# Performance work log

Measured on AMD Instinct MI355X. Metric: run time of the kernel, lower is better.

Reference implementation:

```python
import jax, jax.numpy as jnp
import numpy as np

D, H, W = 96, 160, 160
N_FLOWS = 3
RANGE_FLOW = 0.4


def make_base_grid():
    # torch.meshgrid over arange per dim, stacked: [1, 3, D, H, W], channel order (d, h, w)
    zz, yy, xx = jnp.meshgrid(jnp.arange(D), jnp.arange(H), jnp.arange(W), indexing='ij')
    return jnp.stack([zz, yy, xx]).astype(jnp.float32)[None]


def normalize_grid(g):
    # g: [1,3,D,H,W] voxel coords (d,h,w). Apply 2*(v/(s-1) - 0.5), permute to
    # channels-last and reverse channel order -> (x,y,z) as grid_sample expects.
    scale = jnp.array([2.0 / (D - 1), 2.0 / (H - 1), 2.0 / (W - 1)], jnp.float32).reshape(1, 3, 1, 1, 1)
    g = g * scale - 1.0
    return jnp.moveaxis(g, 1, -1)[..., ::-1]  # [1,D,H,W,3], xyz


def grid_sample_3d(img, grid):
    # Trilinear grid_sample, align_corners=False, zeros padding (torch defaults).
    # img: [N,C,D,H,W]; grid: [N,D,H,W,3] with (x,y,z) in [-1,1].
    N, C, Di, Hi, Wi = img.shape
    x = ((grid[..., 0] + 1.0) * Wi - 1.0) * 0.5
    y = ((grid[..., 1] + 1.0) * Hi - 1.0) * 0.5
    z = ((grid[..., 2] + 1.0) * Di - 1.0) * 0.5
    x0 = jnp.floor(x); y0 = jnp.floor(y); z0 = jnp.floor(z)
    tx = x - x0; ty = y - y0; tz = z - z0
    x0i = x0.astype(jnp.int32); y0i = y0.astype(jnp.int32); z0i = z0.astype(jnp.int32)

    gather = jax.vmap(lambda im, a, b, c: im[:, a, b, c])  # per-batch [C,D,H,W] gather

    out = jnp.zeros((N, C) + x.shape[1:], img.dtype)
    for dz in (0, 1):
        for dy in (0, 1):
            for dx in (0, 1):
                xi = x0i + dx; yi = y0i + dy; zi = z0i + dz
                w = ((tx if dx else 1.0 - tx) * (ty if dy else 1.0 - ty) * (tz if dz else 1.0 - tz))
                valid = ((xi >= 0) & (xi < Wi) & (yi >= 0) & (yi < Hi) & (zi >= 0) & (zi < Di))
                xi = jnp.clip(xi, 0, Wi - 1); yi = jnp.clip(yi, 0, Hi - 1); zi = jnp.clip(zi, 0, Di - 1)
                vals = gather(img, zi, yi, xi)  # [N,C,D,H,W]
                out = out + vals * (w * valid)[:, None]
    return out


def setup_inputs() -> dict:
    key = jax.random.key(0)
    k1, k2, k3 = jax.random.split(key, 3)
    src = jax.random.normal(k1, (1, 1, D, H, W), jnp.float32)
    flow_list = jax.random.normal(k2, (N_FLOWS, 1, 3, D, H, W), jnp.float32)
    final_flow = jax.random.normal(k3, (1, 3, D, H, W), jnp.float32)
    range_flow = jnp.float32(RANGE_FLOW)
    return {"src": src, "flow_list": flow_list, "final_flow": final_flow, "range_flow": range_flow}


def reference(src, flow_list, final_flow, range_flow):
    base = make_base_grid()  # [1,3,D,H,W]
    flows = [flow_list[i] for i in range(flow_list.shape[0])] + [final_flow]
    composed = flows[0]
    warped = composed
    for dvf in flows[1:]:
        grid2 = normalize_grid(base + dvf * range_flow)
        warped = grid_sample_3d(composed, grid2)  # warp running composition by dvf
        composed = warped + dvf
    out_flow = warped + final_flow  # == final composed dvf
    new_locs = normalize_grid(base + composed * range_flow)
    deform_2_img = grid_sample_3d(src, new_locs)
    return (deform_2_img, out_flow)
```

## Files before the change

### kernel.cpp

```cpp
#include <hip/hip_runtime.h>

constexpr int Dd  = 96;
constexpr int Hh  = 160;
constexpr int Ww  = 160;
constexpr int HW  = Hh * Ww;
constexpr int DHW = Dd * HW;

__device__ __forceinline__ float remap_z(float v) { return v * ((float)Dd / (float)(Dd - 1)) - 0.5f; }
__device__ __forceinline__ float remap_y(float v) { return v * ((float)Hh / (float)(Hh - 1)) - 0.5f; }
__device__ __forceinline__ float remap_x(float v) { return v * ((float)Ww / (float)(Ww - 1)) - 0.5f; }

__device__ __forceinline__ void tri_setup(float x, float y, float z,
                                          int off[8], float wgt[8]) {
    float xf = floorf(x), yf = floorf(y), zf = floorf(z);
    float tx = x - xf, ty = y - yf, tz = z - zf;
    int x0 = (int)xf, y0 = (int)yf, z0 = (int)zf;
    float wx[2] = {1.0f - tx, tx};
    float wy[2] = {1.0f - ty, ty};
    float wz[2] = {1.0f - tz, tz};
    int k = 0;
#pragma unroll
    for (int dz = 0; dz < 2; ++dz) {
        int zi = z0 + dz;
        bool vz = (zi >= 0) && (zi < Dd);
        int zc = min(max(zi, 0), Dd - 1);
#pragma unroll
        for (int dy = 0; dy < 2; ++dy) {
            int yi = y0 + dy;
            bool vy = (yi >= 0) && (yi < Hh);
            int yc = min(max(yi, 0), Hh - 1);
#pragma unroll
            for (int dx = 0; dx < 2; ++dx) {
                int xi = x0 + dx;
                bool vx = (xi >= 0) && (xi < Ww);
                int xc = min(max(xi, 0), Ww - 1);
                float w = wz[dz] * wy[dy] * wx[dx];
                wgt[k] = (vx && vy && vz) ? w : 0.0f;
                off[k] = zc * HW + yc * Ww + xc;
                ++k;
            }
        }
    }
}

__global__ __launch_bounds__(256) void pack3to4(
        const float* __restrict__ f, float4* __restrict__ out)
{
    int idx = blockIdx.x * blockDim.x + threadIdx.x;
    if (idx >= DHW) return;
    out[idx] = make_float4(f[idx], f[DHW + idx], f[2 * DHW + idx], 0.0f);
}

template <bool PLANAR_OUT>
__global__ __launch_bounds__(256) void warp_compose4(
        const float4* __restrict__ composed,
        const float* __restrict__ dvf,
        const float* __restrict__ rf_ptr,
        float* __restrict__ outp,
        float4* __restrict__ out4)
{
    int idx = blockIdx.x * blockDim.x + threadIdx.x;
    if (idx >= DHW) return;
    float rf = *rf_ptr;

    int d = idx / HW;
    int rem = idx - d * HW;
    int h = rem / Ww;
    int w = rem - h * Ww;

    float fd = dvf[idx];
    float fh = dvf[DHW + idx];
    float fw = dvf[2 * DHW + idx];

    float z = remap_z((float)d + fd * rf);
    float y = remap_y((float)h + fh * rf);
    float x = remap_x((float)w + fw * rf);

    int off[8]; float wgt[8];
    tri_setup(x, y, z, off, wgt);

    float a0 = 0.0f, a1 = 0.0f, a2 = 0.0f;
#pragma unroll
    for (int k = 0; k < 8; ++k) {
        float4 v = composed[off[k]];
        float wk = wgt[k];
        a0 += wk * v.x;
        a1 += wk * v.y;
        a2 += wk * v.z;
    }
    if (PLANAR_OUT) {
        outp[idx]           = a0 + fd;
        outp[DHW + idx]     = a1 + fh;
        outp[2 * DHW + idx] = a2 + fw;
    } else {
        out4[idx] = make_float4(a0 + fd, a1 + fh, a2 + fw, 0.0f);
    }
}

__global__ __launch_bounds__(256) void warp_src(
        const float* __restrict__ src,
        const float* __restrict__ composed,
        const float* __restrict__ rf_ptr,
        float* __restrict__ out)
{
    int idx = blockIdx.x * blockDim.x + threadIdx.x;
    if (idx >= DHW) return;
    float rf = *rf_ptr;

    int d = idx / HW;
    int rem = idx - d * HW;
    int h = rem / Ww;
    int w = rem - h * Ww;

    float fd = composed[idx];
    float fh = composed[DHW + idx];
    float fw = composed[2 * DHW + idx];

    float z = remap_z((float)d + fd * rf);
    float y = remap_y((float)h + fh * rf);
    float x = remap_x((float)w + fw * rf);

    int off[8]; float wgt[8];
    tri_setup(x, y, z, off, wgt);

    float acc = 0.0f;
#pragma unroll
    for (int k = 0; k < 8; ++k) {
        acc += wgt[k] * src[off[k]];
    }
    out[idx] = acc;
}

extern "C" void kernel_launch(void* const* d_in, const int* in_sizes, int n_in,
                              void* d_out, int out_size, void* d_ws, size_t ws_size,
                              hipStream_t stream) {
    const float* src        = (const float*)d_in[0];
    const float* flow_list  = (const float*)d_in[1];
    const float* final_flow = (const float*)d_in[2];
    const float* rf         = (const float*)d_in[3];

    float* out_img  = (float*)d_out;
    float* out_flow = (float*)d_out + DHW;

    float4* bufA = (float4*)d_ws;
    float4* bufB = bufA + DHW;

    const float* f0 = flow_list;
    const float* f1 = flow_list + 3 * (size_t)DHW;
    const float* f2 = flow_list + 6 * (size_t)DHW;

    dim3 block(256);
    dim3 grid(DHW / 256);

    pack3to4<<<grid, block, 0, stream>>>(f0, bufA);
    warp_compose4<false><<<grid, block, 0, stream>>>(bufA, f1, rf, nullptr, bufB);
    warp_compose4<false><<<grid, block, 0, stream>>>(bufB, f2, rf, nullptr, bufA);
    warp_compose4<true><<<grid, block, 0, stream>>>(bufA, final_flow, rf, out_flow, nullptr);
    warp_src<<<grid, block, 0, stream>>>(src, out_flow, rf, out_img);
}
```

Baseline: 294.5 us.

## Fuse final flow composition with source warp and swizzle block order

Merges the last compose step and the image warp into one kernel, so the composed flow is used from registers instead of being written out and read back, and one launch goes away. Block indices are also remapped so that consecutive workgroups are spread across eight contiguous chunks, likely to balance spatial locality across XCDs and their L2 caches. Bounds checks are dropped, which relies on DHW being a multiple of 256.

```diff
diff --git a/kernel.cpp b/kernel.cpp
--- a/kernel.cpp
+++ b/kernel.cpp
@@ -5,6 +5,12 @@
 constexpr int Ww  = 160;
 constexpr int HW  = Hh * Ww;
 constexpr int DHW = Dd * HW;
+constexpr int NBLK  = DHW / 256;
+constexpr int CHUNK = NBLK / 8;
+
+__device__ __forceinline__ int swz_block(int b) {
+    return (b & 7) * CHUNK + (b >> 3);
+}
 
 __device__ __forceinline__ float remap_z(float v) { return v * ((float)Dd / (float)(Dd - 1)) - 0.5f; }
 __device__ __forceinline__ float remap_y(float v) { return v * ((float)Hh / (float)(Hh - 1)) - 0.5f; }
@@ -47,20 +53,16 @@
         const float* __restrict__ f, float4* __restrict__ out)
 {
     int idx = blockIdx.x * blockDim.x + threadIdx.x;
-    if (idx >= DHW) return;
     out[idx] = make_float4(f[idx], f[DHW + idx], f[2 * DHW + idx], 0.0f);
 }
 
-template <bool PLANAR_OUT>
 __global__ __launch_bounds__(256) void warp_compose4(
         const float4* __restrict__ composed,
         const float* __restrict__ dvf,
         const float* __restrict__ rf_ptr,
-        float* __restrict__ outp,
         float4* __restrict__ out4)
 {
-    int idx = blockIdx.x * blockDim.x + threadIdx.x;
-    if (idx >= DHW) return;
+    int idx = swz_block(blockIdx.x) * 256 + threadIdx.x;
     float rf = *rf_ptr;
 
     int d = idx / HW;
@@ -88,23 +90,18 @@
         a1 += wk * v.y;
         a2 += wk * v.z;
     }
-    if (PLANAR_OUT) {
-        outp[idx]           = a0 + fd;
-        outp[DHW + idx]     = a1 + fh;
-        outp[2 * DHW + idx] = a2 + fw;
-    } else {
-        out4[idx] = make_float4(a0 + fd, a1 + fh, a2 + fw, 0.0f);
-    }
+    out4[idx] = make_float4(a0 + fd, a1 + fh, a2 + fw, 0.0f);
 }
 
-__global__ __launch_bounds__(256) void warp_src(
+__global__ __launch_bounds__(256) void warp_final_fused(
+        const float4* __restrict__ composed2,
+        const float* __restrict__ fflow,
         const float* __restrict__ src,
-        const float* __restrict__ composed,
         const float* __restrict__ rf_ptr,
-        float* __restrict__ out)
+        float* __restrict__ out_flow,
+        float* __restrict__ out_img)
 {
-    int idx = blockIdx.x * blockDim.x + threadIdx.x;
-    if (idx >= DHW) return;
+    int idx = swz_block(blockIdx.x) * 256 + threadIdx.x;
     float rf = *rf_ptr;
 
     int d = idx / HW;
@@ -112,9 +109,9 @@
     int h = rem / Ww;
     int w = rem - h * Ww;
 
-    float fd = composed[idx];
-    float fh = composed[DHW + idx];
-    float fw = composed[2 * DHW + idx];
+    float fd = fflow[idx];
+    float fh = fflow[DHW + idx];
+    float fw = fflow[2 * DHW + idx];
 
     float z = remap_z((float)d + fd * rf);
     float y = remap_y((float)h + fh * rf);
@@ -123,12 +120,31 @@
     int off[8]; float wgt[8];
     tri_setup(x, y, z, off, wgt);
 
+    float a0 = 0.0f, a1 = 0.0f, a2 = 0.0f;
+#pragma unroll
+    for (int k = 0; k < 8; ++k) {
+        float4 v = composed2[off[k]];
+        float wk = wgt[k];
+        a0 += wk * v.x;
+        a1 += wk * v.y;
+        a2 += wk * v.z;
+    }
+    float c0 = a0 + fd, c1 = a1 + fh, c2 = a2 + fw;
+    out_flow[idx]           = c0;
+    out_flow[DHW + idx]     = c1;
+    out_flow[2 * DHW + idx] = c2;
+
+    float z2 = remap_z((float)d + c0 * rf);
+    float y2 = remap_y((float)h + c1 * rf);
+    float x2 = remap_x((float)w + c2 * rf);
+
+    tri_setup(x2, y2, z2, off, wgt);
     float acc = 0.0f;
 #pragma unroll
     for (int k = 0; k < 8; ++k) {
         acc += wgt[k] * src[off[k]];
     }
-    out[idx] = acc;
+    out_img[idx] = acc;
 }
 
 extern "C" void kernel_launch(void* const* d_in, const int* in_sizes, int n_in,
@@ -150,11 +166,11 @@
     const float* f2 = flow_list + 6 * (size_t)DHW;
 
     dim3 block(256);
-    dim3 grid(DHW / 256);
+    dim3 grid(NBLK);
 
     pack3to4<<<grid, block, 0, stream>>>(f0, bufA);
-    warp_compose4<false><<<grid, block, 0, stream>>>(bufA, f1, rf, nullptr, bufB);
-    warp_compose4<false><<<grid, block, 0, stream>>>(bufB, f2, rf, nullptr, bufA);
-    warp_compose4<true><<<grid, block, 0, stream>>>(bufA, final_flow, rf, out_flow, nullptr);
-    warp_src<<<grid, block, 0, stream>>>(src, out_flow, rf, out_img);
+    warp_compose4<<<grid, block, 0, stream>>>(bufA, f1, rf, bufB);
+    warp_compose4<<<grid, block, 0, stream>>>(bufB, f2, rf, bufA);
+    warp_final_fused<<<grid, block, 0, stream>>>(bufA, final_flow, src, rf,
+                                                 out_flow, out_img);
 }
```

New measurement: 278.0 us. 5.6% less time.
